# Kernel tuning notes

Measured on AMD Instinct MI355X. Metric: run time of the kernel, lower is better.

## Reference

```python
import jax, jax.numpy as jnp
import numpy as np

B, N, D, H = 4, 1024, 512, 16
DH = D // H
FACTOR = 0.5 / np.sqrt(DH).astype(np.float32)


def setup_inputs() -> dict:
    key = jax.random.key(0)
    ks = jax.random.split(key, 16)
    w = lambda k, shape: (jax.random.normal(k, shape, dtype=jnp.float32) * 0.02)
    return {
        "H": jax.random.normal(ks[0], (B, N, D), dtype=jnp.float32),
        "V": jax.random.normal(ks[1], (B, N, 3, D), dtype=jnp.float32),
        "D_batch": jax.random.normal(ks[2], (B, N, N), dtype=jnp.float32),
        "rbf_feat": jax.random.normal(ks[3], (1, B, H, N, N), dtype=jnp.float32),
        "H_mask": jax.random.randint(ks[4], (B, N), 0, 2).astype(jnp.int32),
        "Wq": w(ks[5], (4 * D, D)), "bq": w(ks[6], (4 * D,)),
        "Wk": w(ks[7], (4 * D, D)), "bk": w(ks[8], (4 * D,)),
        "Wv": w(ks[9], (D, D)), "bv": w(ks[10], (D,)),
        "Wvv": w(ks[11], (D, D)),
        "Wo": w(ks[12], (D, D)), "bo": w(ks[13], (D,)),
        "Wvo": w(ks[14], (D, D)),
    }


def reference(H, V, D_batch, rbf_feat, H_mask, Wq, bq, Wk, bk, Wv, bv, Wvv, Wo, bo, Wvo):
    b, n, d = H.shape
    h = rbf_feat.shape[2]
    dh = d // h
    # projections
    H_q = (H @ Wq.T + bq).reshape(b, n, h, 4 * dh)
    H_k = (H @ Wk.T + bk).reshape(b, n, h, 4 * dh)
    H_v = (H @ Wv.T + bv).reshape(b, n, h, dh)
    # vector values: [b,n,3,d] -> [b,n,3,h,dh] -> [b,n,h,3,dh] -> [b,n,h,3*dh]
    V_v = jnp.einsum('bncd,ed->bnce', V, Wvv)
    V_v = jnp.swapaxes(V_v.reshape(b, n, 3, h, dh), -2, -3).reshape(b, n, h, 3 * dh)
    V_attn = jnp.concatenate([H_v, V_v], axis=-1)  # [b,n,h,4*dh]
    # additive bias + key mask
    bias = rbf_feat[0] + D_batch[:, None]            # [b,h,n,n]
    mask = (H_mask[:, None, None, :] != 0)           # [b,1,1,n]
    bias = jnp.where(mask, bias, -jnp.inf)
    scores = jnp.einsum('bnhd,bmhd->bhnm', H_q, H_k) * jnp.float32(FACTOR) + bias
    attn = jax.nn.softmax(scores, axis=-1)
    res = jnp.einsum('bhnm,bmhd->bnhd', attn, V_attn)  # [b,n,h,4*dh]
    H_res = res[..., :dh].reshape(b, n, d)
    V_res = jnp.swapaxes(res[..., dh:].reshape(b, n, h, 3, dh), -2, -3).reshape(b, n, 3, d)
    H_o = H_res @ Wo.T + bo
    V_o = jnp.einsum('bncd,ed->bnce', V_res, Wvo)
    return (H_o, V_o)
```

## Files before the change

kernel.cpp:

```cpp
#include <hip/hip_runtime.h>
#include <cmath>

#define FACTOR 0.08838834764831845f

typedef short s16x8 __attribute__((ext_vector_type(8)));
typedef float f32x4 __attribute__((ext_vector_type(4)));
typedef float f32x16 __attribute__((ext_vector_type(16)));
typedef unsigned int u32;

#define KEEP_LOADS() do { asm volatile("" ::: "memory"); __builtin_amdgcn_sched_barrier(0); } while (0)

__device__ __forceinline__ unsigned short f2bf(float x) {
  unsigned int u = __float_as_uint(x);
  u += 0x7FFFu + ((u >> 16) & 1u);
  return (unsigned short)(u >> 16);
}

__device__ __forceinline__ s16x8 pack8(float4 a, float4 b) {
  s16x8 r;
  r[0] = (short)f2bf(a.x); r[1] = (short)f2bf(a.y);
  r[2] = (short)f2bf(a.z); r[3] = (short)f2bf(a.w);
  r[4] = (short)f2bf(b.x); r[5] = (short)f2bf(b.y);
  r[6] = (short)f2bf(b.z); r[7] = (short)f2bf(b.w);
  return r;
}

__device__ __forceinline__ void gload_lds16(const void* g, void* l) {
  __builtin_amdgcn_global_load_lds(
      (const __attribute__((address_space(1))) u32*)g,
      (__attribute__((address_space(3))) u32*)l, 16, 0, 0);
}

template <int CTRL>
__device__ __forceinline__ float dppmax(float x) {
  int y = __builtin_amdgcn_mov_dpp(__float_as_int(x), CTRL, 0xf, 0xf, false);
  return fmaxf(x, __int_as_float(y));
}
template <int CTRL>
__device__ __forceinline__ float dppadd(float x) {
  int y = __builtin_amdgcn_mov_dpp(__float_as_int(x), CTRL, 0xf, 0xf, false);
  return x + __int_as_float(y);
}
__device__ __forceinline__ float swz16(float x) {
  return __int_as_float(__builtin_amdgcn_ds_swizzle(__float_as_int(x), 0x401F));
}
__device__ __forceinline__ float red32max(float x) {
  x = dppmax<0xB1>(x);
  x = dppmax<0x4E>(x);
  x = dppmax<0x141>(x);
  x = dppmax<0x140>(x);
  return fmaxf(x, swz16(x));
}
__device__ __forceinline__ float red32add(float x) {
  x = dppadd<0xB1>(x);
  x = dppadd<0x4E>(x);
  x = dppadd<0x141>(x);
  x = dppadd<0x140>(x);
  return x + swz16(x);
}

__global__ __launch_bounds__(256) void gemm_mfma(
    const float* __restrict__ A, const float* __restrict__ B,
    const float* __restrict__ bias, void* __restrict__ C,
    int M, int N, int K, int mode)
{
  __shared__ unsigned short As[128 * 72];
  __shared__ unsigned short Bs[128 * 72];

  const int tid = threadIdx.x;
  const int w = tid >> 6, lane = tid & 63;
  const int l16 = lane & 15, lg = lane >> 4;
  const int wm = w >> 1, wn = w & 1;
  const int m0 = blockIdx.x * 128;
  const int n0 = blockIdx.y * 128;

  const int sr = tid >> 3;
  const int sc = (tid & 7) * 8;

  float4 ar[4][2], br[4][2];

  auto issue = [&](int k0) {
#pragma unroll
    for (int i = 0; i < 4; ++i) {
      const int rr = i * 32 + sr;
      const float* ap = A + (size_t)(m0 + rr) * K + k0 + sc;
      ar[i][0] = *(const float4*)ap;
      ar[i][1] = *(const float4*)(ap + 4);
      const float* bp;
      if (mode == 5) {
        const int t = n0 + rr;
        const int q3 = t >> 10, n = t & 1023;
        const int bb = q3 / 3, cd = q3 - 3 * bb;
        bp = B + (((size_t)(bb * 1024 + n)) * 3 + cd) * 512 + k0 + sc;
      } else {
        bp = B + (size_t)(n0 + rr) * K + k0 + sc;
      }
      br[i][0] = *(const float4*)bp;
      br[i][1] = *(const float4*)(bp + 4);
    }
  };

  f32x4 acc[4][4];
#pragma unroll
  for (int mt = 0; mt < 4; ++mt)
#pragma unroll
    for (int nt = 0; nt < 4; ++nt)
#pragma unroll
      for (int r = 0; r < 4; ++r) acc[mt][nt][r] = 0.f;

  issue(0);

#pragma unroll 1
  for (int k0 = 0; k0 < K; k0 += 64) {
    __builtin_amdgcn_s_barrier();
#pragma unroll
    for (int i = 0; i < 4; ++i) {
      const int rr = i * 32 + sr;
      *(s16x8*)&As[rr * 72 + sc] = pack8(ar[i][0], ar[i][1]);
      *(s16x8*)&Bs[rr * 72 + sc] = pack8(br[i][0], br[i][1]);
    }
    asm volatile("s_waitcnt lgkmcnt(0)" ::: "memory");
    __builtin_amdgcn_s_barrier();
    if (k0 + 64 < K) issue(k0 + 64);
    KEEP_LOADS();

#pragma unroll
    for (int ks = 0; ks < 2; ++ks) {
      s16x8 af[4], bf[4];
#pragma unroll
      for (int mt = 0; mt < 4; ++mt)
        af[mt] = *(const s16x8*)&As[(wm * 64 + mt * 16 + l16) * 72 + ks * 32 + lg * 8];
#pragma unroll
      for (int nt = 0; nt < 4; ++nt)
        bf[nt] = *(const s16x8*)&Bs[(wn * 64 + nt * 16 + l16) * 72 + ks * 32 + lg * 8];
#pragma unroll
      for (int mt = 0; mt < 4; ++mt)
#pragma unroll
        for (int nt = 0; nt < 4; ++nt)
          acc[mt][nt] = __builtin_amdgcn_mfma_f32_16x16x32_bf16(af[mt], bf[nt], acc[mt][nt], 0, 0, 0);
    }
  }

  const int rbase = m0 + wm * 64;
  const int cbase = n0 + wn * 64;

  if (mode == 0 || mode == 3) {
#pragma unroll
    for (int nt = 0; nt < 4; ++nt) {
      const int c = cbase + nt * 16 + l16;
      const float bb = bias ? bias[c] : 0.f;
#pragma unroll
      for (int mt = 0; mt < 4; ++mt) {
#pragma unroll
        for (int r = 0; r < 4; ++r) {
          const int row = rbase + mt * 16 + lg * 4 + r;
          const float v = acc[mt][nt][r] + bb;
          if (mode == 0) ((float*)C)[(size_t)row * N + c] = v;
          else           ((unsigned short*)C)[(size_t)row * N + c] = f2bf(v);
        }
      }
    }
  } else {
    unsigned short* Cb = (unsigned short*)C;
#pragma unroll
    for (int mt = 0; mt < 4; ++mt) {
#pragma unroll
      for (int r = 0; r < 4; ++r) {
        const int ch = rbase + mt * 16 + lg * 4 + r;
        const float bb = bias ? bias[ch] : 0.f;
        const int h = ch >> 5, dq = ch & 31;
#pragma unroll
        for (int nt = 0; nt < 4; ++nt) {
          const int t = cbase + nt * 16 + l16;
          size_t off;
          if (mode == 4) {
            const int b = t >> 10, n = t & 1023;
            off = (((size_t)(b * 16 + h)) * 128 + dq) * 1024 + n;
          } else {
            const int q3 = t >> 10, n = t & 1023;
            const int b = q3 / 3, cd = q3 - 3 * b;
            off = (((size_t)(b * 16 + h)) * 128 + 32 + cd * 32 + dq) * 1024 + n;
          }
          Cb[off] = f2bf(acc[mt][nt][r] + bb);
        }
      }
    }
  }
}

__global__ __launch_bounds__(256, 2) void attn_mfma(
    const unsigned short* __restrict__ Qg, const unsigned short* __restrict__ Kg,
    const unsigned short* __restrict__ Vtg, const float* __restrict__ rbf,
    const float* __restrict__ Dm, const int* __restrict__ msk,
    float* __restrict__ Hres, float* __restrict__ Vres)
{
  __shared__ unsigned short KsL[2][4096];
  __shared__ unsigned short VtL[2][4096];
  __shared__ unsigned short PsL[4][32 * 40];
  __shared__ int   MsL[1024];
  __shared__ float RbL[128 * 32];
  __shared__ float DbL[128 * 32];

  const int tid  = threadIdx.x;
  const int w    = tid >> 6;
  const int lane = tid & 63;
  const int l32  = lane & 31;
  const int hi   = lane >> 5;

  const int bh = blockIdx.y;
  const int b  = bh >> 4;
  const int h  = bh & 15;
  const int q0 = blockIdx.x * 128 + w * 32;

  s16x8 qf[8];
  {
    const unsigned short* qp = Qg + ((size_t)(b * 1024 + q0 + l32)) * 2048 + h * 128 + hi * 8;
#pragma unroll
    for (int ks = 0; ks < 8; ++ks) qf[ks] = *(const s16x8*)(qp + ks * 16);
  }

  f32x16 acc[4];
  float m_run[16], l_run[16];
#pragma unroll
  for (int dt = 0; dt < 4; ++dt)
#pragma unroll
    for (int r = 0; r < 16; ++r) acc[dt][r] = 0.f;
#pragma unroll
  for (int r = 0; r < 16; ++r) { m_run[r] = -INFINITY; l_run[r] = 0.f; }

  auto issue_kv = [&](int t, int bf) {
    const int m0 = t * 32;
#pragma unroll
    for (int jj = 0; jj < 2; ++jj) {
      const int i = w * 2 + jj;
      gload_lds16(Kg + ((size_t)(b * 1024 + m0 + l32)) * 2048 + h * 128 + (2 * i + hi) * 8,
                  &KsL[bf][i * 512]);
      gload_lds16(Vtg + ((size_t)(bh * 128 + (i >> 1) * 32 + l32)) * 1024 + m0 + ((i & 1) * 2 + hi) * 8,
                  &VtL[bf][i * 512]);
    }
  };

  auto issue_bias = [&](int t) {
    const int m0 = t * 32;
#pragma unroll
    for (int i = 0; i < 4; ++i) {
      const int qq = q0 + i * 8 + (lane >> 3);
      const int ch = (lane & 7) * 4;
      gload_lds16(rbf + ((size_t)bh * 1024 + qq) * 1024 + m0 + ch, &RbL[w * 1024 + i * 256]);
      gload_lds16(Dm  + ((size_t)b  * 1024 + qq) * 1024 + m0 + ch, &DbL[w * 1024 + i * 256]);
    }
  };

  gload_lds16(msk + b * 1024 + w * 256 + lane * 4, &MsL[w * 256]);
  issue_kv(0, 0);
  issue_bias(0);

#pragma unroll 1
  for (int t = 0; t < 32; ++t) {
    const int bf = t & 1;
    const int m0 = t * 32;

    asm volatile("s_waitcnt vmcnt(0)" ::: "memory");
    __builtin_amdgcn_s_barrier();

    if (t < 31) issue_kv(t + 1, bf ^ 1);
    __builtin_amdgcn_sched_barrier(0);

    f32x16 sf;
#pragma unroll
    for (int r = 0; r < 16; ++r) sf[r] = 0.f;
    __builtin_amdgcn_s_setprio(1);
#pragma unroll
    for (int ks = 0; ks < 8; ++ks) {
      const s16x8 kf = *(const s16x8*)&KsL[bf][(ks * 2 + hi) * 256 + l32 * 8];
      sf = __builtin_amdgcn_mfma_f32_32x32x16_bf16(qf[ks], kf, sf, 0, 0, 0);
    }
    __builtin_amdgcn_s_setprio(0);

    const bool on = MsL[m0 + l32] != 0;
    float sv[16];
#pragma unroll
    for (int r = 0; r < 16; ++r) {
      const int ql = (r & 3) + 8 * (r >> 2) + 4 * hi;
      const float bb = RbL[w * 1024 + ql * 32 + l32] + DbL[w * 1024 + ql * 32 + l32];
      sv[r] = on ? fmaf(sf[r], FACTOR, bb) : -INFINITY;
    }
    if (t < 31) issue_bias(t + 1);
    __builtin_amdgcn_sched_barrier(0);

    float tmax[16];
    bool ok = true;
#pragma unroll
    for (int r = 0; r < 16; ++r) {
      tmax[r] = red32max(sv[r]);
      ok = ok && (tmax[r] <= m_run[r] + 8.f);
    }
    if (!__all(ok ? 1 : 0)) {
#pragma unroll
      for (int r = 0; r < 16; ++r) {
        const float mn = fmaxf(m_run[r], tmax[r]);
        const float sc = (mn == m_run[r]) ? 1.f : __expf(m_run[r] - mn);
        m_run[r] = mn;
        l_run[r] *= sc;
#pragma unroll
        for (int dt = 0; dt < 4; ++dt) acc[dt][r] *= sc;
      }
    }
    float psv[16];
#pragma unroll
    for (int r = 0; r < 16; ++r)
      psv[r] = (sv[r] == -INFINITY) ? 0.f : __expf(sv[r] - m_run[r]);
#pragma unroll
    for (int r = 0; r < 16; ++r) l_run[r] += red32add(psv[r]);

#pragma unroll
    for (int r = 0; r < 16; ++r) {
      const int ql = (r & 3) + 8 * (r >> 2) + 4 * hi;
      PsL[w][ql * 40 + l32] = f2bf(psv[r]);
    }
    asm volatile("s_waitcnt lgkmcnt(0)" ::: "memory");
    __builtin_amdgcn_sched_barrier(0);

    const s16x8 pf0 = *(const s16x8*)&PsL[w][l32 * 40 + hi * 8];
    const s16x8 pf1 = *(const s16x8*)&PsL[w][l32 * 40 + 16 + hi * 8];
    __builtin_amdgcn_s_setprio(1);
#pragma unroll
    for (int dt = 0; dt < 4; ++dt) {
      const s16x8 vf0 = *(const s16x8*)&VtL[bf][dt * 1024 + hi * 256 + l32 * 8];
      const s16x8 vf1 = *(const s16x8*)&VtL[bf][dt * 1024 + (2 + hi) * 256 + l32 * 8];
      acc[dt] = __builtin_amdgcn_mfma_f32_32x32x16_bf16(pf0, vf0, acc[dt], 0, 0, 0);
      acc[dt] = __builtin_amdgcn_mfma_f32_32x32x16_bf16(pf1, vf1, acc[dt], 0, 0, 0);
    }
    __builtin_amdgcn_s_setprio(0);
  }

  float inv[16];
#pragma unroll
  for (int r = 0; r < 16; ++r) inv[r] = (l_run[r] > 0.f) ? 1.f / l_run[r] : 0.f;

#pragma unroll
  for (int dt = 0; dt < 4; ++dt) {
#pragma unroll
    for (int r = 0; r < 16; ++r) {
      const int q = q0 + (r & 3) + 8 * (r >> 2) + 4 * hi;
      const float o = acc[dt][r] * inv[r];
      if (dt == 0) {
        Hres[((size_t)(b * 1024 + q)) * 512 + h * 32 + l32] = o;
      } else {
        Vres[(((size_t)(b * 1024 + q)) * 3 + (dt - 1)) * 512 + h * 32 + l32] = o;
      }
    }
  }
}

extern "C" void kernel_launch(void* const* d_in, const int* in_sizes, int n_in,
                              void* d_out, int out_size, void* d_ws, size_t ws_size,
                              hipStream_t stream)
{
  const float* Hp  = (const float*)d_in[0];
  const float* Vp  = (const float*)d_in[1];
  const float* Db  = (const float*)d_in[2];
  const float* rbf = (const float*)d_in[3];
  const int*   Hm  = (const int*)d_in[4];
  const float* Wq  = (const float*)d_in[5];
  const float* bq  = (const float*)d_in[6];
  const float* Wk  = (const float*)d_in[7];
  const float* bk  = (const float*)d_in[8];
  const float* Wv  = (const float*)d_in[9];
  const float* bv  = (const float*)d_in[10];
  const float* Wvv = (const float*)d_in[11];
  const float* Wo  = (const float*)d_in[12];
  const float* bo  = (const float*)d_in[13];
  const float* Wvo = (const float*)d_in[14];
  float* out = (float*)d_out;

  if (ws_size < (size_t)83886080) return;
  unsigned short* Qb = (unsigned short*)d_ws;
  unsigned short* Kb = Qb + 8388608;
  unsigned short* Vt = Kb + 8388608;
  float* Hres = (float*)(Vt + 8388608);
  float* Vres = Hres + 2097152;

  const dim3 blk(256);

  gemm_mfma<<<dim3(32, 16), blk, 0, stream>>>(Hp, Wq, bq, Qb, 4096, 2048, 512, 3);
  gemm_mfma<<<dim3(32, 16), blk, 0, stream>>>(Hp, Wk, bk, Kb, 4096, 2048, 512, 3);
  gemm_mfma<<<dim3(4, 32),  blk, 0, stream>>>(Wv, Hp, bv, Vt, 512, 4096, 512, 4);
  gemm_mfma<<<dim3(4, 96),  blk, 0, stream>>>(Wvv, Vp, nullptr, Vt, 512, 12288, 512, 5);

  attn_mfma<<<dim3(8, 64), blk, 0, stream>>>(Qb, Kb, Vt, rbf, Db, Hm, Hres, Vres);

  gemm_mfma<<<dim3(32, 4), blk, 0, stream>>>(Hres, Wo, bo, out, 4096, 512, 512, 0);
  gemm_mfma<<<dim3(96, 4), blk, 0, stream>>>(Vres, Wvo, nullptr, out + 2097152, 12288, 512, 512, 0);
}
```

Measured before the change: 290.2 us.

## Transpose score tile through LDS so softmax reductions stay within each lane

Softmax row reductions used to run as cross-lane DPP/swizzle reductions for each of the 16 accumulator rows. The score tile is now transposed through a small padded LDS buffer, in two halves, so each lane holds 16 elements of one query row. Max and sum then become per-lane loops plus a single shuffle, and the running max and sum collapse to scalars. The PV MFMA operands are swapped so the output is transposed to match, which changes the output store pattern to strided columns. The cost is extra LDS round trips and waits per tile, less coalesced final stores, and a lane-pair shared max that may trigger rescaling more often.

```diff
diff --git a/kernel.cpp b/kernel.cpp
--- a/kernel.cpp
+++ b/kernel.cpp
@@ -29,34 +29,6 @@
   __builtin_amdgcn_global_load_lds(
       (const __attribute__((address_space(1))) u32*)g,
       (__attribute__((address_space(3))) u32*)l, 16, 0, 0);
-}
-
-template <int CTRL>
-__device__ __forceinline__ float dppmax(float x) {
-  int y = __builtin_amdgcn_mov_dpp(__float_as_int(x), CTRL, 0xf, 0xf, false);
-  return fmaxf(x, __int_as_float(y));
-}
-template <int CTRL>
-__device__ __forceinline__ float dppadd(float x) {
-  int y = __builtin_amdgcn_mov_dpp(__float_as_int(x), CTRL, 0xf, 0xf, false);
-  return x + __int_as_float(y);
-}
-__device__ __forceinline__ float swz16(float x) {
-  return __int_as_float(__builtin_amdgcn_ds_swizzle(__float_as_int(x), 0x401F));
-}
-__device__ __forceinline__ float red32max(float x) {
-  x = dppmax<0xB1>(x);
-  x = dppmax<0x4E>(x);
-  x = dppmax<0x141>(x);
-  x = dppmax<0x140>(x);
-  return fmaxf(x, swz16(x));
-}
-__device__ __forceinline__ float red32add(float x) {
-  x = dppadd<0xB1>(x);
-  x = dppadd<0x4E>(x);
-  x = dppadd<0x141>(x);
-  x = dppadd<0x140>(x);
-  return x + swz16(x);
 }
 
 __global__ __launch_bounds__(256) void gemm_mfma(
@@ -196,10 +168,10 @@
 {
   __shared__ unsigned short KsL[2][4096];
   __shared__ unsigned short VtL[2][4096];
-  __shared__ unsigned short PsL[4][32 * 40];
   __shared__ int   MsL[1024];
   __shared__ float RbL[128 * 32];
   __shared__ float DbL[128 * 32];
+  __shared__ float SsL[4][32 * 18];
 
   const int tid  = threadIdx.x;
   const int w    = tid >> 6;
@@ -220,13 +192,11 @@
   }
 
   f32x16 acc[4];
-  float m_run[16], l_run[16];
+  float m_run = -INFINITY, l_run = 0.f;
 #pragma unroll
   for (int dt = 0; dt < 4; ++dt)
 #pragma unroll
     for (int r = 0; r < 16; ++r) acc[dt][r] = 0.f;
-#pragma unroll
-  for (int r = 0; r < 16; ++r) { m_run[r] = -INFINITY; l_run[r] = 0.f; }
 
   auto issue_kv = [&](int t, int bf) {
     const int m0 = t * 32;
@@ -285,69 +255,107 @@
       const float bb = RbL[w * 1024 + ql * 32 + l32] + DbL[w * 1024 + ql * 32 + l32];
       sv[r] = on ? fmaf(sf[r], FACTOR, bb) : -INFINITY;
     }
+    asm volatile("s_waitcnt lgkmcnt(0)" ::: "memory");
+    __builtin_amdgcn_sched_barrier(0);
     if (t < 31) issue_bias(t + 1);
     __builtin_amdgcn_sched_barrier(0);
 
-    float tmax[16];
-    bool ok = true;
-#pragma unroll
-    for (int r = 0; r < 16; ++r) {
-      tmax[r] = red32max(sv[r]);
-      ok = ok && (tmax[r] <= m_run[r] + 8.f);
-    }
+    float s[16];
+    if (l32 < 16) {
+#pragma unroll
+      for (int r = 0; r < 16; ++r) {
+        const int ql = (r & 3) + 8 * (r >> 2) + 4 * hi;
+        SsL[w][ql * 18 + l32] = sv[r];
+      }
+    }
+    asm volatile("s_waitcnt lgkmcnt(0)" ::: "memory");
+    __builtin_amdgcn_sched_barrier(0);
+    if (hi == 0) {
+#pragma unroll
+      for (int j = 0; j < 16; ++j) s[j] = SsL[w][l32 * 18 + j];
+    }
+    __builtin_amdgcn_sched_barrier(0);
+    if (l32 >= 16) {
+#pragma unroll
+      for (int r = 0; r < 16; ++r) {
+        const int ql = (r & 3) + 8 * (r >> 2) + 4 * hi;
+        SsL[w][ql * 18 + (l32 - 16)] = sv[r];
+      }
+    }
+    asm volatile("s_waitcnt lgkmcnt(0)" ::: "memory");
+    __builtin_amdgcn_sched_barrier(0);
+    if (hi == 1) {
+#pragma unroll
+      for (int j = 0; j < 16; ++j) s[j] = SsL[w][l32 * 18 + j];
+    }
+    __builtin_amdgcn_sched_barrier(0);
+
+    float mx = s[0];
+#pragma unroll
+    for (int j = 1; j < 16; ++j) mx = fmaxf(mx, s[j]);
+    const float tmax = fmaxf(mx, __shfl_xor(mx, 32));
+
+    const bool ok = (tmax <= m_run + 8.f);
     if (!__all(ok ? 1 : 0)) {
-#pragma unroll
-      for (int r = 0; r < 16; ++r) {
-        const float mn = fmaxf(m_run[r], tmax[r]);
-        const float sc = (mn == m_run[r]) ? 1.f : __expf(m_run[r] - mn);
-        m_run[r] = mn;
-        l_run[r] *= sc;
-#pragma unroll
-        for (int dt = 0; dt < 4; ++dt) acc[dt][r] *= sc;
-      }
-    }
+      const float mn = fmaxf(m_run, tmax);
+      const float sc = (mn == m_run) ? 1.f : __expf(m_run - mn);
+      m_run = mn;
+      l_run *= sc;
+#pragma unroll
+      for (int dt = 0; dt < 4; ++dt)
+#pragma unroll
+        for (int r = 0; r < 16; ++r) acc[dt][r] *= sc;
+    }
+
     float psv[16];
-#pragma unroll
-    for (int r = 0; r < 16; ++r)
-      psv[r] = (sv[r] == -INFINITY) ? 0.f : __expf(sv[r] - m_run[r]);
-#pragma unroll
-    for (int r = 0; r < 16; ++r) l_run[r] += red32add(psv[r]);
-
-#pragma unroll
-    for (int r = 0; r < 16; ++r) {
-      const int ql = (r & 3) + 8 * (r >> 2) + 4 * hi;
-      PsL[w][ql * 40 + l32] = f2bf(psv[r]);
+    float rs = 0.f;
+#pragma unroll
+    for (int j = 0; j < 16; ++j) {
+      psv[j] = (s[j] == -INFINITY) ? 0.f : __expf(s[j] - m_run);
+      rs += psv[j];
+    }
+    l_run += rs;
+
+    {
+      u32* Pw = (u32*)&SsL[w][0];
+#pragma unroll
+      for (int j = 0; j < 8; ++j) {
+        const u32 word = (u32)f2bf(psv[2 * j]) | ((u32)f2bf(psv[2 * j + 1]) << 16);
+        Pw[l32 * 18 + hi * 8 + j] = word;
+      }
     }
     asm volatile("s_waitcnt lgkmcnt(0)" ::: "memory");
     __builtin_amdgcn_sched_barrier(0);
 
-    const s16x8 pf0 = *(const s16x8*)&PsL[w][l32 * 40 + hi * 8];
-    const s16x8 pf1 = *(const s16x8*)&PsL[w][l32 * 40 + 16 + hi * 8];
+    const unsigned short* Pr = (const unsigned short*)&SsL[w][0];
+    const s16x8 pf0 = *(const s16x8*)&Pr[l32 * 36 + hi * 8];
+    const s16x8 pf1 = *(const s16x8*)&Pr[l32 * 36 + 16 + hi * 8];
+
     __builtin_amdgcn_s_setprio(1);
 #pragma unroll
     for (int dt = 0; dt < 4; ++dt) {
       const s16x8 vf0 = *(const s16x8*)&VtL[bf][dt * 1024 + hi * 256 + l32 * 8];
       const s16x8 vf1 = *(const s16x8*)&VtL[bf][dt * 1024 + (2 + hi) * 256 + l32 * 8];
-      acc[dt] = __builtin_amdgcn_mfma_f32_32x32x16_bf16(pf0, vf0, acc[dt], 0, 0, 0);
-      acc[dt] = __builtin_amdgcn_mfma_f32_32x32x16_bf16(pf1, vf1, acc[dt], 0, 0, 0);
+      acc[dt] = __builtin_amdgcn_mfma_f32_32x32x16_bf16(vf0, pf0, acc[dt], 0, 0, 0);
+      acc[dt] = __builtin_amdgcn_mfma_f32_32x32x16_bf16(vf1, pf1, acc[dt], 0, 0, 0);
     }
     __builtin_amdgcn_s_setprio(0);
   }
 
-  float inv[16];
-#pragma unroll
-  for (int r = 0; r < 16; ++r) inv[r] = (l_run[r] > 0.f) ? 1.f / l_run[r] : 0.f;
-
+  const float lt = l_run + __shfl_xor(l_run, 32);
+  const float inv = (lt > 0.f) ? 1.f / lt : 0.f;
+
+  const int q = q0 + l32;
 #pragma unroll
   for (int dt = 0; dt < 4; ++dt) {
 #pragma unroll
     for (int r = 0; r < 16; ++r) {
-      const int q = q0 + (r & 3) + 8 * (r >> 2) + 4 * hi;
-      const float o = acc[dt][r] * inv[r];
+      const int dloc = (r & 3) + 8 * (r >> 2) + 4 * hi;
+      const float o = acc[dt][r] * inv;
       if (dt == 0) {
-        Hres[((size_t)(b * 1024 + q)) * 512 + h * 32 + l32] = o;
+        Hres[((size_t)(b * 1024 + q)) * 512 + h * 32 + dloc] = o;
       } else {
-        Vres[(((size_t)(b * 1024 + q)) * 3 + (dt - 1)) * 512 + h * 32 + l32] = o;
+        Vres[(((size_t)(b * 1024 + q)) * 3 + (dt - 1)) * 512 + h * 32 + dloc] = o;
       }
     }
   }
```

After: 275.2 us. 1.05x faster.
